# Performance work log

Measured on AMD Instinct MI355X. Metric: run time of the kernel, lower is better.

Reference implementation:

```python
import jax, jax.numpy as jnp
import numpy as np

DIM = 1024
NUM_HEADS = 16
HEAD_DIM = DIM // NUM_HEADS


def setup_inputs() -> dict:
    key = jax.random.key(0)
    ks = jax.random.split(key, 9)
    s = 1.0 / np.sqrt(DIM)
    x = jax.random.normal(ks[0], (2, 2048, DIM), dtype=jnp.float32)
    Wq = jax.random.uniform(ks[1], (DIM, DIM), jnp.float32, -s, s)
    bq = jax.random.uniform(ks[2], (DIM,), jnp.float32, -s, s)
    Wk = jax.random.uniform(ks[3], (DIM, DIM), jnp.float32, -s, s)
    bk = jax.random.uniform(ks[4], (DIM,), jnp.float32, -s, s)
    Wv = jax.random.uniform(ks[5], (DIM, DIM), jnp.float32, -s, s)
    bv = jax.random.uniform(ks[6], (DIM,), jnp.float32, -s, s)
    Wo = jax.random.uniform(ks[7], (DIM, DIM), jnp.float32, -s, s)
    bo = jax.random.uniform(ks[8], (DIM,), jnp.float32, -s, s)
    return {"x": x, "Wq": Wq, "bq": bq, "Wk": Wk, "bk": bk,
            "Wv": Wv, "bv": bv, "Wo": Wo, "bo": bo}


def reference(x, Wq, bq, Wk, bk, Wv, bv, Wo, bo):
    B, S, _ = x.shape
    # projections (torch Linear: y = x @ W.T + b); split heads -> [B, H, S, Dh]
    def split(y):
        return y.reshape(B, S, NUM_HEADS, HEAD_DIM).transpose(0, 2, 1, 3)
    q = split(x @ Wq.T + bq)
    k = split(x @ Wk.T + bk)
    v = split(x @ Wv.T + bv)
    scale = 1.0 / np.sqrt(HEAD_DIM).astype(np.float32)
    scores = jnp.einsum('bhqd,bhkd->bhqk', q, k) * scale  # [B,H,S,S]
    attn = jax.nn.softmax(scores, axis=-1)
    ctx = jnp.einsum('bhqk,bhkd->bhqd', attn, v)  # [B,H,S,Dh]
    ctx = ctx.transpose(0, 2, 1, 3).reshape(B, S, DIM)
    return ctx @ Wo.T + bo
```

## Files before the change

### kernel.cpp

```cpp
#include <hip/hip_runtime.h>
#include <hip/hip_bf16.h>
#include <math.h>

#define DIMSZ 1024
#define NHEAD 16
#define HDIM 64
#define BATCH 2
#define SEQ 2048
#define NROWS (BATCH * SEQ)

#define QSCALE 0.18033688011112042592f

typedef __attribute__((ext_vector_type(8))) _Float16 f16x8;
typedef __attribute__((ext_vector_type(2))) __fp16 fp16x2;
typedef __attribute__((ext_vector_type(4))) float f32x4;

__device__ __forceinline__ int swz(int m) { return (m ^ (m >> 2)) & 3; }

__device__ __forceinline__ ushort f2h(float x) {
    union { _Float16 h; ushort u; } cv;
    cv.h = (_Float16)x;
    return cv.u;
}

__device__ __forceinline__ unsigned pkrtz(float a, float b) {
    union { fp16x2 v; unsigned u; } c;
    c.v = __builtin_amdgcn_cvt_pkrtz(a, b);
    return c.u;
}

__device__ __forceinline__ void gld16(const void* g, void* l) {
    __builtin_amdgcn_global_load_lds((const __attribute__((address_space(1))) void*)g,
                                     (__attribute__((address_space(3))) void*)l,
                                     16, 0, 0);
}

__global__ __launch_bounds__(256) void convert_all(
    const float* __restrict__ x,
    const float* __restrict__ Wq, const float* __restrict__ Wk,
    const float* __restrict__ Wv, const float* __restrict__ Wo,
    ushort* __restrict__ Xh, ushort* __restrict__ Wh, ushort* __restrict__ Woh)
{
    const int b = blockIdx.x;
    const float* src;
    ushort* dst;
    size_t off;
    if (b < 2048)      { src = x;  dst = Xh;             off = (size_t)b * 2048; }
    else if (b < 2560) { src = Wq; dst = Wh;             off = (size_t)(b - 2048) * 2048; }
    else if (b < 3072) { src = Wk; dst = Wh + (1 << 20); off = (size_t)(b - 2560) * 2048; }
    else if (b < 3584) { src = Wv; dst = Wh + 2 * (1 << 20); off = (size_t)(b - 3072) * 2048; }
    else               { src = Wo; dst = Woh;            off = (size_t)(b - 3584) * 2048; }

    const size_t i = off + (size_t)threadIdx.x * 8;
    const float4 f0 = *(const float4*)&src[i];
    const float4 f1 = *(const float4*)&src[i + 4];
    uint4 hv;
    hv.x = (unsigned)f2h(f0.x) | ((unsigned)f2h(f0.y) << 16);
    hv.y = (unsigned)f2h(f0.z) | ((unsigned)f2h(f0.w) << 16);
    hv.z = (unsigned)f2h(f1.x) | ((unsigned)f2h(f1.y) << 16);
    hv.w = (unsigned)f2h(f1.z) | ((unsigned)f2h(f1.w) << 16);
    *(uint4*)&dst[i] = hv;
}

__global__ __launch_bounds__(256, 3) void qkv_gemm(
    const ushort* __restrict__ Xh,
    const ushort* __restrict__ Wh,
    const float* __restrict__ bq, const float* __restrict__ bk,
    const float* __restrict__ bv,
    ushort* __restrict__ Qb, ushort* __restrict__ Kb, ushort* __restrict__ Vt)
{
    __shared__ __align__(16) ushort smem[17408];

    const int tid = threadIdx.x;
    const int wave = tid >> 6;
    const int lane = tid & 63;
    const int lm = lane & 15;
    const int lq = lane >> 4;
    const int wy = wave >> 1;
    const int wx = wave & 1;
    const int m0 = blockIdx.x * 128;
    const int nbase = blockIdx.y * 128;

    const int c = tid & 3;
    const int r0 = tid >> 2;
    const int g = c ^ swz(r0 & 15);
    const ushort* gah = Xh + (size_t)(m0 + r0) * DIMSZ + g * 8;
    const ushort* gbh = Wh + (size_t)(nbase + r0) * DIMSZ + g * 8;
    const int wofs = wave * 512;

    const int fo = lm * 32 + (((lq ^ swz(lm)) & 3) << 3);
    int aofs[4], bofs[4];
#pragma unroll
    for (int i = 0; i < 4; ++i) {
        aofs[i] = (wy * 64 + i * 16) * 32 + fo;
        bofs[i] = (wx * 64 + i * 16) * 32 + fo;
    }

    f32x4 acc[4][4] = {};

    {
        gld16(gah, smem + wofs);                 gld16(gah + 64 * DIMSZ, smem + 2048 + wofs);
        gld16(gbh, smem + 4096 + wofs);          gld16(gbh + 64 * DIMSZ, smem + 6144 + wofs);
    }

    for (int kk = 0; kk < 32; ++kk) {
        __syncthreads();

        const ushort* Ah = smem;
        const ushort* Bh = smem + 4096;

        f16x8 ahf[4], bhf[4];
#pragma unroll
        for (int i = 0; i < 4; ++i) {
            ahf[i] = *(const f16x8*)&Ah[aofs[i]];
            bhf[i] = *(const f16x8*)&Bh[bofs[i]];
        }

        __syncthreads();

        if (kk + 1 < 32) {
            const int k0 = (kk + 1) * 32;
            gld16(gah + k0, smem + wofs);                 gld16(gah + 64 * DIMSZ + k0, smem + 2048 + wofs);
            gld16(gbh + k0, smem + 4096 + wofs);          gld16(gbh + 64 * DIMSZ + k0, smem + 6144 + wofs);
        }

#pragma unroll
        for (int i = 0; i < 4; ++i)
#pragma unroll
            for (int j = 0; j < 4; ++j)
                acc[i][j] = __builtin_amdgcn_mfma_f32_16x16x32_f16(ahf[i], bhf[j], acc[i][j], 0, 0, 0);
    }

    const int mat = blockIdx.y >> 3;
    const float* bias = (mat == 0) ? bq : (mat == 1) ? bk : bv;
    const int nloc0 = (blockIdx.y & 7) * 128;
    const int b = m0 >> 11;
    const int s0 = m0 & (SEQ - 1);
    ushort* sf = smem;

    __syncthreads();

    if (mat == 2) {
#pragma unroll
        for (int j = 0; j < 4; ++j) {
            const int nc = nloc0 + wx * 64 + j * 16 + lm;
            const float bb = bias[nc];
            const int d = j * 16 + lm;
#pragma unroll
            for (int i = 0; i < 4; ++i) {
                const int ss = wy * 64 + (i >> 1) * 32 + lq * 8 + (i & 1) * 4;
                ushort4 pk;
                pk.x = f2h(acc[i][j][0] + bb);
                pk.y = f2h(acc[i][j][1] + bb);
                pk.z = f2h(acc[i][j][2] + bb);
                pk.w = f2h(acc[i][j][3] + bb);
                *(ushort4*)&sf[(wx * 64 + d) * 136 + ss] = pk;
            }
        }
        __syncthreads();
#pragma unroll
        for (int p = 0; p < 8; ++p) {
            const int idx = p * 256 + tid;
            const int row = idx >> 4;
            const int hh = row >> 6;
            const int d = row & 63;
            const int sseg = (idx & 15) * 8;
            const uint4 v = *(const uint4*)&sf[row * 136 + sseg];
            const int hg = (nloc0 >> 6) + hh;
            *(uint4*)&Vt[((size_t)(b * NHEAD + hg) * HDIM + d) * SEQ + s0 + sseg] = v;
        }
    } else {
        ushort* dst = (mat == 0) ? Qb : Kb;
        const float sc = (mat == 0) ? QSCALE : 1.0f;
#pragma unroll
        for (int j = 0; j < 4; ++j) {
            const int col = wx * 64 + j * 16 + lm;
            const float bb = bias[nloc0 + col];
#pragma unroll
            for (int i = 0; i < 4; ++i) {
                const int rbase = wy * 64 + i * 16 + lq * 4;
#pragma unroll
                for (int rr = 0; rr < 4; ++rr)
                    sf[(rbase + rr) * 136 + col] = f2h((acc[i][j][rr] + bb) * sc);
            }
        }
        __syncthreads();
#pragma unroll
        for (int p = 0; p < 8; ++p) {
            const int idx = p * 256 + tid;
            const int row = idx >> 4;
            const int seg = idx & 15;
            const uint4 v = *(const uint4*)&sf[row * 136 + seg * 8];
            const int nc0 = nloc0 + seg * 8;
            const int h = nc0 >> 6;
            const int d = nc0 & 63;
            *(uint4*)&dst[((size_t)(b * NHEAD + h) * SEQ + s0 + row) * HDIM + d] = v;
        }
    }
}

__global__ __launch_bounds__(256, 2) void flash_attn_mfma(
    const ushort* __restrict__ Qb, const ushort* __restrict__ Kb,
    const ushort* __restrict__ Vt, ushort* __restrict__ CTXh)
{
    __shared__ __align__(16) ushort Ks[2][8192];
    __shared__ __align__(16) ushort Vs[2][8192];

    const int tid = threadIdx.x;
    const int w = tid >> 6;
    const int l = tid & 63;
    const int lm = l & 15;
    const int lq = l >> 4;
    const int q0 = blockIdx.x * 128;
    const int bh = blockIdx.y;
    const int NCH = SEQ / 128;

    const int ch0 = (bh >> 4) * 8;

    const ushort* Kg = Kb + (size_t)bh * SEQ * HDIM;
    const ushort* Vg = Vt + (size_t)bh * HDIM * SEQ;

    const int sr8 = l >> 3;
    const int sg_ = (l & 7) ^ (sr8 & 7);

    f16x8 qf[2][2];
#pragma unroll
    for (int rt = 0; rt < 2; ++rt)
#pragma unroll
        for (int kt = 0; kt < 2; ++kt)
            qf[rt][kt] = *(const f16x8*)&Qb[((size_t)bh * SEQ + q0 + w * 32 + rt * 16 + lm) * HDIM + kt * 32 + lq * 8];

    int kbase[2], vbase[4];
#pragma unroll
    for (int kt = 0; kt < 2; ++kt)
        kbase[kt] = lm * 64 + (((kt * 4 + lq) ^ (lm & 7)) << 3);
#pragma unroll
    for (int kt2 = 0; kt2 < 4; ++kt2)
        vbase[kt2] = (kt2 >> 1) * 4096 + lm * 64 + ((((kt2 & 1) * 4 + lq) ^ (lm & 7)) << 3);

    f16x8 vones;
#pragma unroll
    for (int i = 0; i < 8; ++i) vones[i] = (_Float16)1.0f;

    f32x4 o[2][4] = {};
    f32x4 lacc[2] = {};

    {
        const int kc0 = ch0 * 128;
#pragma unroll
        for (int p = 0; p < 2; ++p) {
            const int kr = kc0 + p * 64 + w * 16 + sr8;
            gld16(Kg + (size_t)kr * HDIM + sg_ * 8,        &Ks[0][0] + p * 4096 + w * 1024);
            gld16(Kg + (size_t)(kr + 8) * HDIM + sg_ * 8,  &Ks[0][0] + p * 4096 + w * 1024 + 512);
            const int vr = w * 16 + sr8;
            gld16(Vg + (size_t)vr * SEQ + kc0 + p * 64 + sg_ * 8,       &Vs[0][0] + p * 4096 + w * 1024);
            gld16(Vg + (size_t)(vr + 8) * SEQ + kc0 + p * 64 + sg_ * 8, &Vs[0][0] + p * 4096 + w * 1024 + 512);
        }
    }

    for (int it = 0; it < NCH; ++it) {
        __syncthreads();

        if (it + 1 < NCH) {
            const int kc = ((ch0 + it + 1) & (NCH - 1)) * 128;
            ushort* kb_n = &Ks[(it + 1) & 1][0];
            ushort* vb_n = &Vs[(it + 1) & 1][0];
#pragma unroll
            for (int p = 0; p < 2; ++p) {
                const int kr = kc + p * 64 + w * 16 + sr8;
                gld16(Kg + (size_t)kr * HDIM + sg_ * 8,        kb_n + p * 4096 + w * 1024);
                gld16(Kg + (size_t)(kr + 8) * HDIM + sg_ * 8,  kb_n + p * 4096 + w * 1024 + 512);
                const int vr = w * 16 + sr8;
                gld16(Vg + (size_t)vr * SEQ + kc + p * 64 + sg_ * 8,       vb_n + p * 4096 + w * 1024);
                gld16(Vg + (size_t)(vr + 8) * SEQ + kc + p * 64 + sg_ * 8, vb_n + p * 4096 + w * 1024 + 512);
            }
        }

        const ushort* kb = &Ks[it & 1][0];
        const ushort* vb = &Vs[it & 1][0];

        f32x4 st[2][8] = {};
        __builtin_amdgcn_s_setprio(1);
#pragma unroll
        for (int ct = 0; ct < 8; ++ct)
#pragma unroll
            for (int kt = 0; kt < 2; ++kt) {
                const f16x8 kf = *(const f16x8*)&kb[ct * 1024 + kbase[kt]];
                st[0][ct] = __builtin_amdgcn_mfma_f32_16x16x32_f16(kf, qf[0][kt], st[0][ct], 0, 0, 0);
                st[1][ct] = __builtin_amdgcn_mfma_f32_16x16x32_f16(kf, qf[1][kt], st[1][ct], 0, 0, 0);
            }
        __builtin_amdgcn_s_setprio(0);

#pragma unroll
        for (int rt = 0; rt < 2; ++rt)
#pragma unroll
            for (int ct = 0; ct < 8; ++ct)
#pragma unroll
                for (int r = 0; r < 4; ++r)
                    st[rt][ct][r] = __builtin_amdgcn_exp2f(st[rt][ct][r]);

        f16x8 pf[2][4];
#pragma unroll
        for (int rt = 0; rt < 2; ++rt)
#pragma unroll
            for (int kt2 = 0; kt2 < 4; ++kt2) {
                union { f16x8 v; unsigned u[4]; } pk;
#pragma unroll
                for (int t = 0; t < 2; ++t) {
                    pk.u[t * 2 + 0] = pkrtz(st[rt][kt2 * 2 + t][0], st[rt][kt2 * 2 + t][1]);
                    pk.u[t * 2 + 1] = pkrtz(st[rt][kt2 * 2 + t][2], st[rt][kt2 * 2 + t][3]);
                }
                pf[rt][kt2] = pk.v;
            }

        __builtin_amdgcn_s_setprio(1);
#pragma unroll
        for (int kt2 = 0; kt2 < 4; ++kt2) {
            lacc[0] = __builtin_amdgcn_mfma_f32_16x16x32_f16(pf[0][kt2], vones, lacc[0], 0, 0, 0);
            lacc[1] = __builtin_amdgcn_mfma_f32_16x16x32_f16(pf[1][kt2], vones, lacc[1], 0, 0, 0);
        }

#pragma unroll
        for (int dt = 0; dt < 4; ++dt)
#pragma unroll
            for (int kt2 = 0; kt2 < 4; ++kt2) {
                const f16x8 vf = *(const f16x8*)&vb[dt * 1024 + vbase[kt2]];
                o[0][dt] = __builtin_amdgcn_mfma_f32_16x16x32_f16(pf[0][kt2], vf, o[0][dt], 0, 0, 0);
                o[1][dt] = __builtin_amdgcn_mfma_f32_16x16x32_f16(pf[1][kt2], vf, o[1][dt], 0, 0, 0);
            }
        __builtin_amdgcn_s_setprio(0);
    }

    const int b = bh >> 4;
    const int h = bh & 15;
#pragma unroll
    for (int rt = 0; rt < 2; ++rt)
#pragma unroll
    for (int r = 0; r < 4; ++r) {
        const float lr = 1.0f / lacc[rt][r];
        const int srow2 = q0 + w * 32 + rt * 16 + lq * 4 + r;
        const size_t base = ((size_t)b * SEQ + srow2) * DIMSZ + h * HDIM;
#pragma unroll
        for (int dt = 0; dt < 4; ++dt)
            CTXh[base + dt * 16 + lm] = f2h(o[rt][dt][r] * lr);
    }
}

__global__ __launch_bounds__(256) void oproj_gemm(
    const ushort* __restrict__ Ah_g, const ushort* __restrict__ Bh_g,
    const float* __restrict__ bias, float* __restrict__ out)
{
    __shared__ __align__(16) ushort smem[6144];

    const int tid = threadIdx.x;
    const int wave = tid >> 6;
    const int lane = tid & 63;
    const int lm = lane & 15;
    const int lq = lane >> 4;
    const int wy = wave >> 1;
    const int wx = wave & 1;
    const int m0 = blockIdx.x * 64;
    const int n0 = blockIdx.y * 128;

    const int c = tid & 3;
    const int r0 = tid >> 2;
    const int g = c ^ swz(r0 & 15);
    const ushort* gah = Ah_g + (size_t)(m0 + r0) * DIMSZ + g * 8;
    const ushort* gbh = Bh_g + (size_t)(n0 + r0) * DIMSZ + g * 8;
    const int wofs = wave * 512;

    const int fo = lm * 32 + (((lq ^ swz(lm)) & 3) << 3);
    int aofs[2], bofs[4];
#pragma unroll
    for (int i = 0; i < 2; ++i) aofs[i] = (wy * 32 + i * 16) * 32 + fo;
#pragma unroll
    for (int j = 0; j < 4; ++j) bofs[j] = (wx * 64 + j * 16) * 32 + fo;

    f32x4 acc[2][4] = {};

    {
        gld16(gah, smem + wofs);
        gld16(gbh, smem + 2048 + wofs);   gld16(gbh + 64 * DIMSZ, smem + 4096 + wofs);
    }

    for (int kk = 0; kk < 32; ++kk) {
        __syncthreads();

        f16x8 ahf[2], bhf[4];
#pragma unroll
        for (int i = 0; i < 2; ++i) ahf[i] = *(const f16x8*)&smem[aofs[i]];
#pragma unroll
        for (int j = 0; j < 4; ++j) bhf[j] = *(const f16x8*)&smem[2048 + bofs[j]];

        __syncthreads();

        if (kk + 1 < 32) {
            const int k0 = (kk + 1) * 32;
            gld16(gah + k0, smem + wofs);
            gld16(gbh + k0, smem + 2048 + wofs);   gld16(gbh + 64 * DIMSZ + k0, smem + 4096 + wofs);
        }

#pragma unroll
        for (int i = 0; i < 2; ++i)
#pragma unroll
            for (int j = 0; j < 4; ++j)
                acc[i][j] = __builtin_amdgcn_mfma_f32_16x16x32_f16(ahf[i], bhf[j], acc[i][j], 0, 0, 0);
    }

#pragma unroll
    for (int j = 0; j < 4; ++j) {
        const int nc = n0 + wx * 64 + j * 16 + lm;
        const float bb = bias[nc];
#pragma unroll
        for (int i = 0; i < 2; ++i) {
            const int mb = m0 + wy * 32 + i * 16 + lq * 4;
#pragma unroll
            for (int rr = 0; rr < 4; ++rr)
                out[(size_t)(mb + rr) * DIMSZ + nc] = acc[i][j][rr] + bb;
        }
    }
}

extern "C" void kernel_launch(void* const* d_in, const int* in_sizes, int n_in,
                              void* d_out, int out_size, void* d_ws, size_t ws_size,
                              hipStream_t stream)
{
    const float* x  = (const float*)d_in[0];
    const float* Wq = (const float*)d_in[1];
    const float* bq = (const float*)d_in[2];
    const float* Wk = (const float*)d_in[3];
    const float* bk = (const float*)d_in[4];
    const float* Wv = (const float*)d_in[5];
    const float* bv = (const float*)d_in[6];
    const float* Wo = (const float*)d_in[7];
    const float* bo = (const float*)d_in[8];
    float* out = (float*)d_out;

    const size_t elems = (size_t)NROWS * DIMSZ;
    ushort* Qb   = (ushort*)d_ws;
    ushort* Kb   = Qb + elems;
    ushort* Vt   = Kb + elems;
    ushort* CTXh = Vt + elems;
    ushort* Wh   = CTXh + elems;
    ushort* Woh  = Wh + 3 * (1 << 20);
    ushort* Xh   = CTXh;

    convert_all<<<4096, 256, 0, stream>>>(x, Wq, Wk, Wv, Wo, Xh, Wh, Woh);

    qkv_gemm<<<dim3(32, 24), 256, 0, stream>>>(Xh, Wh, bq, bk, bv, Qb, Kb, Vt);

    flash_attn_mfma<<<dim3(SEQ / 128, BATCH * NHEAD), 256, 0, stream>>>(Qb, Kb, Vt, CTXh);

    oproj_gemm<<<dim3(64, 8), 256, 0, stream>>>(CTXh, Woh, bo, out);
}
```

Measured before the change: 177.9 us.

## Double the K-tile depth to 64 in QKV and output projection GEMMs

Both projection GEMMs now stage 64-wide K slices per iteration instead of 32. This halves the loop trip count and the number of barrier pairs, and it replaces the 4-chunk swizzle with an 8-chunk XOR swizzle for the wider rows. The second half of the MFMA work overlaps with the next tile's async global-to-LDS loads. In exchange the kernels use more LDS per block, which may reduce occupancy, and the LDS address math is more involved.

```diff
diff --git a/kernel.cpp b/kernel.cpp
--- a/kernel.cpp
+++ b/kernel.cpp
@@ -14,8 +14,6 @@
 typedef __attribute__((ext_vector_type(8))) _Float16 f16x8;
 typedef __attribute__((ext_vector_type(2))) __fp16 fp16x2;
 typedef __attribute__((ext_vector_type(4))) float f32x4;
-
-__device__ __forceinline__ int swz(int m) { return (m ^ (m >> 2)) & 3; }
 
 __device__ __forceinline__ ushort f2h(float x) {
     union { _Float16 h; ushort u; } cv;
@@ -81,54 +79,69 @@
     const int m0 = blockIdx.x * 128;
     const int nbase = blockIdx.y * 128;
 
-    const int c = tid & 3;
-    const int r0 = tid >> 2;
-    const int g = c ^ swz(r0 & 15);
+    const int c = tid & 7;
+    const int r0 = tid >> 3;
+    const int g = c ^ (r0 & 7);
     const ushort* gah = Xh + (size_t)(m0 + r0) * DIMSZ + g * 8;
     const ushort* gbh = Wh + (size_t)(nbase + r0) * DIMSZ + g * 8;
-    const int wofs = wave * 512;
-
-    const int fo = lm * 32 + (((lq ^ swz(lm)) & 3) << 3);
-    int aofs[4], bofs[4];
-#pragma unroll
-    for (int i = 0; i < 4; ++i) {
-        aofs[i] = (wy * 64 + i * 16) * 32 + fo;
-        bofs[i] = (wx * 64 + i * 16) * 32 + fo;
-    }
+    const int tofs = tid * 8;
+
+    int aofs[4][2], bofs[4][2];
+#pragma unroll
+    for (int i = 0; i < 4; ++i)
+#pragma unroll
+        for (int kt = 0; kt < 2; ++kt) {
+            const int slot = ((kt * 4 + lq) ^ (lm & 7)) << 3;
+            aofs[i][kt] = (wy * 64 + i * 16 + lm) * 64 + slot;
+            bofs[i][kt] = 8192 + (wx * 64 + i * 16 + lm) * 64 + slot;
+        }
 
     f32x4 acc[4][4] = {};
 
-    {
-        gld16(gah, smem + wofs);                 gld16(gah + 64 * DIMSZ, smem + 2048 + wofs);
-        gld16(gbh, smem + 4096 + wofs);          gld16(gbh + 64 * DIMSZ, smem + 6144 + wofs);
-    }
-
-    for (int kk = 0; kk < 32; ++kk) {
-        __syncthreads();
-
-        const ushort* Ah = smem;
-        const ushort* Bh = smem + 4096;
-
-        f16x8 ahf[4], bhf[4];
+#pragma unroll
+    for (int gg = 0; gg < 4; ++gg) {
+        gld16(gah + gg * 32 * DIMSZ, smem + gg * 2048 + tofs);
+        gld16(gbh + gg * 32 * DIMSZ, smem + 8192 + gg * 2048 + tofs);
+    }
+
+    for (int kk = 0; kk < 16; ++kk) {
+        __syncthreads();
+
+        f16x8 a0[4], b0[4];
 #pragma unroll
         for (int i = 0; i < 4; ++i) {
-            ahf[i] = *(const f16x8*)&Ah[aofs[i]];
-            bhf[i] = *(const f16x8*)&Bh[bofs[i]];
-        }
-
-        __syncthreads();
-
-        if (kk + 1 < 32) {
-            const int k0 = (kk + 1) * 32;
-            gld16(gah + k0, smem + wofs);                 gld16(gah + 64 * DIMSZ + k0, smem + 2048 + wofs);
-            gld16(gbh + k0, smem + 4096 + wofs);          gld16(gbh + 64 * DIMSZ + k0, smem + 6144 + wofs);
-        }
-
+            a0[i] = *(const f16x8*)&smem[aofs[i][0]];
+            b0[i] = *(const f16x8*)&smem[bofs[i][0]];
+        }
 #pragma unroll
         for (int i = 0; i < 4; ++i)
 #pragma unroll
             for (int j = 0; j < 4; ++j)
-                acc[i][j] = __builtin_amdgcn_mfma_f32_16x16x32_f16(ahf[i], bhf[j], acc[i][j], 0, 0, 0);
+                acc[i][j] = __builtin_amdgcn_mfma_f32_16x16x32_f16(a0[i], b0[j], acc[i][j], 0, 0, 0);
+
+        f16x8 a1[4], b1[4];
+#pragma unroll
+        for (int i = 0; i < 4; ++i) {
+            a1[i] = *(const f16x8*)&smem[aofs[i][1]];
+            b1[i] = *(const f16x8*)&smem[bofs[i][1]];
+        }
+
+        __syncthreads();
+
+        if (kk + 1 < 16) {
+            const int k0 = (kk + 1) * 64;
+#pragma unroll
+            for (int gg = 0; gg < 4; ++gg) {
+                gld16(gah + gg * 32 * DIMSZ + k0, smem + gg * 2048 + tofs);
+                gld16(gbh + gg * 32 * DIMSZ + k0, smem + 8192 + gg * 2048 + tofs);
+            }
+        }
+
+#pragma unroll
+        for (int i = 0; i < 4; ++i)
+#pragma unroll
+            for (int j = 0; j < 4; ++j)
+                acc[i][j] = __builtin_amdgcn_mfma_f32_16x16x32_f16(a1[i], b1[j], acc[i][j], 0, 0, 0);
     }
 
     const int mat = blockIdx.y >> 3;
@@ -350,7 +363,7 @@
     const ushort* __restrict__ Ah_g, const ushort* __restrict__ Bh_g,
     const float* __restrict__ bias, float* __restrict__ out)
 {
-    __shared__ __align__(16) ushort smem[6144];
+    __shared__ __align__(16) ushort smem[12288];
 
     const int tid = threadIdx.x;
     const int wave = tid >> 6;
@@ -362,49 +375,71 @@
     const int m0 = blockIdx.x * 64;
     const int n0 = blockIdx.y * 128;
 
-    const int c = tid & 3;
-    const int r0 = tid >> 2;
-    const int g = c ^ swz(r0 & 15);
+    const int c = tid & 7;
+    const int r0 = tid >> 3;
+    const int g = c ^ (r0 & 7);
     const ushort* gah = Ah_g + (size_t)(m0 + r0) * DIMSZ + g * 8;
     const ushort* gbh = Bh_g + (size_t)(n0 + r0) * DIMSZ + g * 8;
-    const int wofs = wave * 512;
-
-    const int fo = lm * 32 + (((lq ^ swz(lm)) & 3) << 3);
-    int aofs[2], bofs[4];
-#pragma unroll
-    for (int i = 0; i < 2; ++i) aofs[i] = (wy * 32 + i * 16) * 32 + fo;
-#pragma unroll
-    for (int j = 0; j < 4; ++j) bofs[j] = (wx * 64 + j * 16) * 32 + fo;
+    const int tofs = tid * 8;
+
+    int aofs[2][2], bofs[4][2];
+#pragma unroll
+    for (int kt = 0; kt < 2; ++kt) {
+        const int slot = ((kt * 4 + lq) ^ (lm & 7)) << 3;
+#pragma unroll
+        for (int i = 0; i < 2; ++i)
+            aofs[i][kt] = (wy * 32 + i * 16 + lm) * 64 + slot;
+#pragma unroll
+        for (int j = 0; j < 4; ++j)
+            bofs[j][kt] = 4096 + (wx * 64 + j * 16 + lm) * 64 + slot;
+    }
 
     f32x4 acc[2][4] = {};
 
     {
-        gld16(gah, smem + wofs);
-        gld16(gbh, smem + 2048 + wofs);   gld16(gbh + 64 * DIMSZ, smem + 4096 + wofs);
-    }
-
-    for (int kk = 0; kk < 32; ++kk) {
-        __syncthreads();
-
-        f16x8 ahf[2], bhf[4];
-#pragma unroll
-        for (int i = 0; i < 2; ++i) ahf[i] = *(const f16x8*)&smem[aofs[i]];
-#pragma unroll
-        for (int j = 0; j < 4; ++j) bhf[j] = *(const f16x8*)&smem[2048 + bofs[j]];
-
-        __syncthreads();
-
-        if (kk + 1 < 32) {
-            const int k0 = (kk + 1) * 32;
-            gld16(gah + k0, smem + wofs);
-            gld16(gbh + k0, smem + 2048 + wofs);   gld16(gbh + 64 * DIMSZ + k0, smem + 4096 + wofs);
-        }
-
+        gld16(gah, smem + tofs);
+        gld16(gah + 32 * DIMSZ, smem + 2048 + tofs);
+#pragma unroll
+        for (int gg = 0; gg < 4; ++gg)
+            gld16(gbh + gg * 32 * DIMSZ, smem + 4096 + gg * 2048 + tofs);
+    }
+
+    for (int kk = 0; kk < 16; ++kk) {
+        __syncthreads();
+
+        f16x8 a0[2], b0[4];
+#pragma unroll
+        for (int i = 0; i < 2; ++i) a0[i] = *(const f16x8*)&smem[aofs[i][0]];
+#pragma unroll
+        for (int j = 0; j < 4; ++j) b0[j] = *(const f16x8*)&smem[bofs[j][0]];
 #pragma unroll
         for (int i = 0; i < 2; ++i)
 #pragma unroll
             for (int j = 0; j < 4; ++j)
-                acc[i][j] = __builtin_amdgcn_mfma_f32_16x16x32_f16(ahf[i], bhf[j], acc[i][j], 0, 0, 0);
+                acc[i][j] = __builtin_amdgcn_mfma_f32_16x16x32_f16(a0[i], b0[j], acc[i][j], 0, 0, 0);
+
+        f16x8 a1[2], b1[4];
+#pragma unroll
+        for (int i = 0; i < 2; ++i) a1[i] = *(const f16x8*)&smem[aofs[i][1]];
+#pragma unroll
+        for (int j = 0; j < 4; ++j) b1[j] = *(const f16x8*)&smem[bofs[j][1]];
+
+        __syncthreads();
+
+        if (kk + 1 < 16) {
+            const int k0 = (kk + 1) * 64;
+            gld16(gah + k0, smem + tofs);
+            gld16(gah + 32 * DIMSZ + k0, smem + 2048 + tofs);
+#pragma unroll
+            for (int gg = 0; gg < 4; ++gg)
+                gld16(gbh + gg * 32 * DIMSZ + k0, smem + 4096 + gg * 2048 + tofs);
+        }
+
+#pragma unroll
+        for (int i = 0; i < 2; ++i)
+#pragma unroll
+            for (int j = 0; j < 4; ++j)
+                acc[i][j] = __builtin_amdgcn_mfma_f32_16x16x32_f16(a1[i], b1[j], acc[i][j], 0, 0, 0);
     }
 
 #pragma unroll
```

After: 175.3 us. Within noise of the previous version (-1.5%).
